# Kernel optimization log

Hardware: AMD Instinct MI355X
Metric: run time of the kernel (lower is better)

## Reference

```python
import jax, jax.numpy as jnp
import numpy as np

NUM_CLASSES = 80
STRIDE = 8
IMG_SIZE = 640
BOX_W, OBJ_W, CLS_W = 7.5, 1.0, 0.5
ANCHORS = jnp.array([[10.0, 13.0], [16.0, 30.0], [33.0, 23.0]], dtype=jnp.float32)
EPS_IOU = 1e-9
EPS_CIOU = 1e-7


def setup_inputs() -> dict:
    key = jax.random.key(0)
    k1, k2, k3 = jax.random.split(key, 3)
    B, na, H, W, D = 16, 3, 80, 80, 5 + NUM_CLASSES
    N = 48  # objects per image
    p_raw = jax.random.normal(k1, (B, na, H, W, D), dtype=jnp.float32)
    labels_xywh = jax.random.uniform(k2, (B, N, 4), dtype=jnp.float32)  # normalized (xc,yc,w,h)
    labels_cls = jax.random.randint(k3, (B, N), 0, NUM_CLASSES, dtype=jnp.int32)
    return {"p_raw": p_raw, "labels_xywh": labels_xywh, "labels_cls": labels_cls}


def _assign_targets(labels_cls, labels_xywh, B, na, H, W):
    lab = labels_xywh * IMG_SIZE  # [B,N,4] in pixels
    gx, gy, gw, gh = lab[..., 0], lab[..., 1], lab[..., 2], lab[..., 3]
    gi_idx = jnp.clip(gx / STRIDE, 0, W - 0.001).astype(jnp.int32)  # [B,N]
    gj_idx = jnp.clip(gy / STRIDE, 0, H - 0.001).astype(jnp.int32)
    a_wh = ANCHORS / STRIDE  # [na,2] anchors in grid units
    gtw, gth = gw / STRIDE, gh / STRIDE
    inter = jnp.minimum(gtw[..., None], a_wh[:, 0]) * jnp.minimum(gth[..., None], a_wh[:, 1])
    union = gtw[..., None] * gth[..., None] + a_wh[:, 0] * a_wh[:, 1] - inter + EPS_IOU
    best_a = jnp.argmax(inter / union, axis=-1).astype(jnp.int32)  # [B,N]

    # 3x3 neighborhood offsets (di over x, dj over y), matching torch loop order
    offs = jnp.array([(di, dj) for di in (-1, 0, 1) for dj in (-1, 0, 1)], dtype=jnp.int32)  # [9,2]
    bidx = jnp.arange(B, dtype=jnp.int32)

    tobj = jnp.zeros((B, na, H, W), dtype=jnp.float32)
    tcls = jnp.zeros((B, na, H, W, NUM_CLASSES), dtype=jnp.float32)
    tbox = jnp.zeros((B, na, H, W, 4), dtype=jnp.float32)

    def step(carry, x):
        tobj, tcls, tbox = carry
        a, gi, gj, c, box = x  # a,gi,gj,c: [B]; box: [B,4]
        ii = jnp.clip(gi[:, None] + offs[None, :, 0], 0, W - 1)  # [B,9]
        jj = jnp.clip(gj[:, None] + offs[None, :, 1], 0, H - 1)  # [B,9]
        b9 = jnp.broadcast_to(bidx[:, None], (B, 9))
        a9 = jnp.broadcast_to(a[:, None], (B, 9))
        c9 = jnp.broadcast_to(c[:, None], (B, 9))
        tobj = tobj.at[b9, a9, jj, ii].set(1.0)
        tcls = tcls.at[b9, a9, jj, ii, c9].set(1.0)
        tbox = tbox.at[b9, a9, jj, ii].set(jnp.broadcast_to(box[:, None, :], (B, 9, 4)))
        return (tobj, tcls, tbox), None

    xs = (best_a.T, gi_idx.T, gj_idx.T, labels_cls.T, jnp.swapaxes(lab, 0, 1))
    (tobj, tcls, tbox), _ = jax.lax.scan(step, (tobj, tcls, tbox), xs)
    return tobj, tcls, tbox


def _ciou(pred, tgt):
    # pred, tgt: [..., 4] (xc, yc, w, h) in pixels
    px, py, pw, ph = pred[..., 0], pred[..., 1], pred[..., 2], pred[..., 3]
    gx, gy, gw, gh = tgt[..., 0], tgt[..., 1], tgt[..., 2], tgt[..., 3]
    px1, py1, px2, py2 = px - pw / 2, py - ph / 2, px + pw / 2, py + ph / 2
    gx1, gy1, gx2, gy2 = gx - gw / 2, gy - gh / 2, gx + gw / 2, gy + gh / 2
    iw = jnp.clip(jnp.minimum(px2, gx2) - jnp.maximum(px1, gx1), 0)
    ih = jnp.clip(jnp.minimum(py2, gy2) - jnp.maximum(py1, gy1), 0)
    inter = iw * ih
    area_p = jnp.clip(px2 - px1, 0) * jnp.clip(py2 - py1, 0)
    area_g = jnp.clip(gx2 - gx1, 0) * jnp.clip(gy2 - gy1, 0)
    union = area_p + area_g - inter + EPS_CIOU
    iou = inter / union
    cw = jnp.clip(jnp.maximum(px2, gx2) - jnp.minimum(px1, gx1), 0)
    ch = jnp.clip(jnp.maximum(py2, gy2) - jnp.minimum(py1, gy1), 0)
    c2 = cw * cw + ch * ch + EPS_CIOU
    rho2 = (px - gx) ** 2 + (py - gy) ** 2
    v = (4.0 / (np.pi ** 2)) * (jnp.arctan(gw / (gh + EPS_CIOU)) - jnp.arctan(pw / (ph + EPS_CIOU))) ** 2
    alpha = jax.lax.stop_gradient(v / (1 - iou + v + EPS_CIOU))
    return 1 - (iou - rho2 / c2 - alpha * v)


def _bce_logits(x, t):
    # stable binary cross-entropy with logits: softplus(x) - t*x
    return jax.nn.softplus(x) - t * x


def reference(p_raw, labels_xywh, labels_cls):
    B, na, H, W, D = p_raw.shape
    ag = ANCHORS / STRIDE  # anchors in grid units
    px = jax.nn.sigmoid(p_raw[..., 0])
    py = jax.nn.sigmoid(p_raw[..., 1])
    pw = jnp.exp(p_raw[..., 2]) * ag[:, 0][None, :, None, None]
    ph = jnp.exp(p_raw[..., 3]) * ag[:, 1][None, :, None, None]
    logits_obj = p_raw[..., 4]
    logits_cls = p_raw[..., 5:]

    gyv, gxv = jnp.meshgrid(jnp.arange(H, dtype=jnp.float32), jnp.arange(W, dtype=jnp.float32), indexing='ij')
    gx = (gxv[None, None] + px) * STRIDE
    gy = (gyv[None, None] + py) * STRIDE
    pxywh = jnp.stack([gx, gy, pw * STRIDE, ph * STRIDE], -1)  # [B,na,H,W,4]

    tobj, tcls, tbox = _assign_targets(labels_cls, labels_xywh, B, na, H, W)
    pos = tobj > 0.5
    n_pos = jnp.maximum(jnp.sum(pos), 1).astype(jnp.float32)

    ciou = _ciou(pxywh, tbox)  # [B,na,H,W]
    l_box = jnp.sum(jnp.where(pos, ciou, 0.0)) / n_pos
    l_obj = jnp.mean(_bce_logits(logits_obj, tobj))
    bce_cls = _bce_logits(logits_cls, tcls)  # [B,na,H,W,nc]
    l_cls = jnp.sum(jnp.where(pos[..., None], bce_cls, 0.0)) / (n_pos * NUM_CLASSES)

    total = BOX_W * l_box + OBJ_W * l_obj + CLS_W * l_cls
    return total
```

## Files before the change

### kernel.cpp

```cpp
#include <hip/hip_runtime.h>

#define NC    80
#define B_    16
#define NA    3
#define HW    80
#define D_    85
#define NLAB  48
#define NCELL  (B_*NA*HW*HW)
#define OBJBLK 300
#define POSBLK (B_*108)
#define NBLK_T (OBJBLK+POSBLK)

__device__ __forceinline__ float softplusf(float x) {
    return fmaxf(x, 0.f) + log1pf(expf(-fabsf(x)));
}
__device__ __forceinline__ int clampi(int v, int lo, int hi) {
    return min(max(v, lo), hi);
}

__global__ __launch_bounds__(256) void k_main(const float* __restrict__ p,
                                              const float* __restrict__ lx,
                                              const int*   __restrict__ lc,
                                              float* __restrict__ opart,
                                              float* __restrict__ ppart) {
    int t = threadIdx.x, bid = blockIdx.x;
    int lane = t & 63, wid = t >> 6;
    __shared__ float r4[4][4];

    if (bid < OBJBLK) {
        int base = bid * 1024;
        const float* a0 = p + (size_t)(base + t      ) * D_ + 4;
        const float* a1 = p + (size_t)(base + t + 256) * D_ + 4;
        const float* a2 = p + (size_t)(base + t + 512) * D_ + 4;
        const float* a3 = p + (size_t)(base + t + 768) * D_ + 4;
        float x0 = *a0;
        float x1 = *a1;
        float x2 = *a2;
        float x3 = *a3;
        float s = (softplusf(x0) + softplusf(x1)) + (softplusf(x2) + softplusf(x3));
        #pragma unroll
        for (int o = 32; o; o >>= 1) s += __shfl_xor(s, o);
        if (lane == 0) r4[wid][0] = s;
        __syncthreads();
        if (t == 0) opart[bid] = r4[0][0] + r4[1][0] + r4[2][0] + r4[3][0];
        return;
    }

    int pb = bid - OBJBLK;
    int b  = pb / 108;

    __shared__ float Lgx[NLAB], Lgy[NLAB], Lgw[NLAB], Lgh[NLAB];
    __shared__ int   Lgi[NLAB], Lgj[NLAB], La[NLAB], Lc[NLAB];

    if (t < NLAB) {
        float4 L = ((const float4*)lx)[b * NLAB + t];
        float gx = L.x * 640.f, gy = L.y * 640.f;
        float gw = L.z * 640.f, gh = L.w * 640.f;
        Lgx[t] = gx; Lgy[t] = gy; Lgw[t] = gw; Lgh[t] = gh;
        Lgi[t] = (int)fminf(fmaxf(gx * 0.125f, 0.f), 79.999f);
        Lgj[t] = (int)fminf(fmaxf(gy * 0.125f, 0.f), 79.999f);
        float gtw = gw * 0.125f, gth = gh * 0.125f;
        const float aw[3] = {1.25f, 2.0f, 4.125f};
        const float ah[3] = {1.625f, 3.75f, 2.875f};
        int a = 0; float best = -1.f;
        #pragma unroll
        for (int k = 0; k < 3; k++) {
            float inter = fminf(gtw, aw[k]) * fminf(gth, ah[k]);
            float uni   = gtw * gth + aw[k] * ah[k] - inter + 1e-9f;
            float r = inter / uni;
            if (r > best) { best = r; a = k; }
        }
        La[t] = a;
        Lc[t] = lc[b * NLAB + t];
    }
    __syncthreads();

    int cand = (pb % 108) * 4 + wid;
    int n = cand / 9, off = cand % 9;
    int gi = Lgi[n], gj = Lgj[n], a = La[n];
    int ii = clampi(gi + off / 3 - 1, 0, 79);
    int jj = clampi(gj + off % 3 - 1, 0, 79);

    bool viol = false;
    if (lane < 9) {
        if (lane < off) {
            int i2 = clampi(gi + lane / 3 - 1, 0, 79);
            int j2 = clampi(gj + lane % 3 - 1, 0, 79);
            viol = (i2 == ii) && (j2 == jj);
        }
    } else {
        int n2 = n + 1 + (lane - 9);
        if (n2 < NLAB && La[n2] == a) {
            int g2 = Lgi[n2], h2 = Lgj[n2];
            viol = ii >= max(g2 - 1, 0) && ii <= min(g2 + 1, 79) &&
                   jj >= max(h2 - 1, 0) && jj <= min(h2 + 1, 79);
        }
    }
    bool own = (__ballot(viol) == 0ull);

    float box = 0.f, cls = 0.f, xc = 0.f, npf = 0.f;
    if (own) {
        int cell = ((b * NA + a) * HW + jj) * HW + ii;
        const float* pc = p + (size_t)cell * D_;
        int c = Lc[n];

        float x = pc[5 + lane];
        float cs = softplusf(x) - ((lane == c) ? x : 0.f);
        if (lane < 16) {
            float x2 = pc[69 + lane];
            cs += softplusf(x2) - ((lane + 64 == c) ? x2 : 0.f);
        }
        #pragma unroll
        for (int o = 32; o; o >>= 1) cs += __shfl_xor(cs, o);

        if (lane == 0) {
            npf = 1.f;
            cls = cs;
            xc  = pc[4];

            float awv = (a == 0) ? 10.f : ((a == 1) ? 16.f : 33.f);
            float ahv = (a == 0) ? 13.f : ((a == 1) ? 30.f : 23.f);
            float p0 = pc[0], p1 = pc[1], p2 = pc[2], p3 = pc[3];
            float sx = 1.f / (1.f + expf(-p0));
            float sy = 1.f / (1.f + expf(-p1));
            float px = ((float)ii + sx) * 8.f;
            float py = ((float)jj + sy) * 8.f;
            float pw = expf(p2) * awv;
            float ph = expf(p3) * ahv;

            float gx = Lgx[n], gy = Lgy[n], gw = Lgw[n], gh = Lgh[n];

            float px1 = px - pw * 0.5f, px2 = px + pw * 0.5f;
            float py1 = py - ph * 0.5f, py2 = py + ph * 0.5f;
            float gx1 = gx - gw * 0.5f, gx2 = gx + gw * 0.5f;
            float gy1 = gy - gh * 0.5f, gy2 = gy + gh * 0.5f;

            float iw = fmaxf(fminf(px2, gx2) - fmaxf(px1, gx1), 0.f);
            float ih = fmaxf(fminf(py2, gy2) - fmaxf(py1, gy1), 0.f);
            float inter = iw * ih;
            float ap = fmaxf(px2 - px1, 0.f) * fmaxf(py2 - py1, 0.f);
            float ag = fmaxf(gx2 - gx1, 0.f) * fmaxf(gy2 - gy1, 0.f);
            float uni = ap + ag - inter + 1e-7f;
            float iou = inter / uni;

            float cw = fmaxf(fmaxf(px2, gx2) - fminf(px1, gx1), 0.f);
            float ch = fmaxf(fmaxf(py2, gy2) - fminf(py1, gy1), 0.f);
            float c2 = cw * cw + ch * ch + 1e-7f;
            float rho2 = (px - gx) * (px - gx) + (py - gy) * (py - gy);

            float dv = atanf(gw / (gh + 1e-7f)) - atanf(pw / (ph + 1e-7f));
            float v = 0.40528473456935108577f * dv * dv;
            float alpha = v / (1.f - iou + v + 1e-7f);
            box = 1.f - (iou - rho2 / c2 - alpha * v);
        }
    }

    if (lane == 0) { r4[wid][0] = box; r4[wid][1] = cls; r4[wid][2] = xc; r4[wid][3] = npf; }
    __syncthreads();
    if (t == 0) {
        float4 o;
        o.x = r4[0][0] + r4[1][0] + r4[2][0] + r4[3][0];
        o.y = r4[0][1] + r4[1][1] + r4[2][1] + r4[3][1];
        o.z = r4[0][2] + r4[1][2] + r4[2][2] + r4[3][2];
        o.w = r4[0][3] + r4[1][3] + r4[2][3] + r4[3][3];
        ((float4*)ppart)[pb] = o;
    }
}

__global__ __launch_bounds__(256) void k_fin(const float* __restrict__ opart,
                                             const float* __restrict__ ppart,
                                             float* __restrict__ out) {
    int t = threadIdx.x, lane = t & 63, wid = t >> 6;
    float o = 0.f, box = 0.f, cls = 0.f, xc = 0.f, np = 0.f;
    if (t < OBJBLK) o = opart[t];
    #pragma unroll
    for (int k = 0; k < 7; k++) {
        int i = t + k * 256;
        if (i < POSBLK) {
            float4 v = ((const float4*)ppart)[i];
            box += v.x; cls += v.y; xc += v.z; np += v.w;
        }
    }
    #pragma unroll
    for (int s = 32; s; s >>= 1) {
        o   += __shfl_xor(o,   s);
        box += __shfl_xor(box, s);
        cls += __shfl_xor(cls, s);
        xc  += __shfl_xor(xc,  s);
        np  += __shfl_xor(np,  s);
    }
    __shared__ float r[4][5];
    if (lane == 0) { r[wid][0]=o; r[wid][1]=box; r[wid][2]=cls; r[wid][3]=xc; r[wid][4]=np; }
    __syncthreads();
    if (t == 0) {
        float O  = r[0][0] + r[1][0] + r[2][0] + r[3][0];
        float Bx = r[0][1] + r[1][1] + r[2][1] + r[3][1];
        float Cl = r[0][2] + r[1][2] + r[2][2] + r[3][2];
        float Xc = r[0][3] + r[1][3] + r[2][3] + r[3][3];
        float Np = r[0][4] + r[1][4] + r[2][4] + r[3][4];
        float npos = fmaxf(Np, 1.f);
        out[0] = 7.5f * Bx / npos
               + (O - Xc) / (float)NCELL
               + 0.5f * Cl / (npos * (float)NC);
    }
}

extern "C" void kernel_launch(void* const* d_in, const int* in_sizes, int n_in,
                              void* d_out, int out_size, void* d_ws, size_t ws_size,
                              hipStream_t stream) {
    const float* p  = (const float*)d_in[0];
    const float* lx = (const float*)d_in[1];
    const int*   lc = (const int*)d_in[2];
    float*       out = (float*)d_out;

    float* opart = (float*)d_ws;
    float* ppart = (float*)((char*)d_ws + 8192);

    k_main<<<NBLK_T, 256, 0, stream>>>(p, lx, lc, opart, ppart);
    k_fin<<<1, 256, 0, stream>>>(opart, ppart, out);
}
```

Baseline: 21.40 us.

## Fuse final reduction into main kernel via atomics and last-block finish

Removes the separate finalize kernel. Blocks now accumulate partial sums with global atomics: a double accumulator for the objectness term and float accumulators for box, class, xc and positive count. A counter lets the last block compute the output. Positive-candidate blocks are also reduced from 1728 to 432, each warp handling four candidates in a loop. This trades one kernel launch for a memset plus atomic contention, adds float-atomic order nondeterminism, and makes blocks less parallel.

```diff
diff --git a/kernel.cpp b/kernel.cpp
--- a/kernel.cpp
+++ b/kernel.cpp
@@ -8,7 +8,7 @@
 #define NLAB  48
 #define NCELL  (B_*NA*HW*HW)
 #define OBJBLK 300
-#define POSBLK (B_*108)
+#define POSBLK 432
 #define NBLK_T (OBJBLK+POSBLK)
 
 __device__ __forceinline__ float softplusf(float x) {
@@ -21,11 +21,14 @@
 __global__ __launch_bounds__(256) void k_main(const float* __restrict__ p,
                                               const float* __restrict__ lx,
                                               const int*   __restrict__ lc,
-                                              float* __restrict__ opart,
-                                              float* __restrict__ ppart) {
+                                              double* __restrict__ accd,
+                                              float*  __restrict__ accf,
+                                              int*    __restrict__ cnt,
+                                              float*  __restrict__ out) {
     int t = threadIdx.x, bid = blockIdx.x;
     int lane = t & 63, wid = t >> 6;
-    __shared__ float r4[4][4];
+
+    bool depok = false;
 
     if (bid < OBJBLK) {
         int base = bid * 1024;
@@ -37,171 +40,158 @@
         float x1 = *a1;
         float x2 = *a2;
         float x3 = *a3;
-        float s = (softplusf(x0) + softplusf(x1)) + (softplusf(x2) + softplusf(x3));
+        double s = (double)softplusf(x0) + (double)softplusf(x1)
+                 + (double)softplusf(x2) + (double)softplusf(x3);
         #pragma unroll
         for (int o = 32; o; o >>= 1) s += __shfl_xor(s, o);
-        if (lane == 0) r4[wid][0] = s;
+        __shared__ double wd[4];
+        if (lane == 0) wd[wid] = s;
         __syncthreads();
-        if (t == 0) opart[bid] = r4[0][0] + r4[1][0] + r4[2][0] + r4[3][0];
-        return;
+        if (t == 0) {
+            double s4 = wd[0] + wd[1] + wd[2] + wd[3];
+            double od = atomicAdd(accd, s4);
+            depok = (od == od);
+        }
+    } else {
+        int pb = bid - OBJBLK;
+        int b  = pb / 27, sub = pb % 27;
+
+        __shared__ float Lgx[NLAB], Lgy[NLAB], Lgw[NLAB], Lgh[NLAB];
+        __shared__ int   Lgi[NLAB], Lgj[NLAB], La[NLAB], Lc[NLAB];
+
+        if (t < NLAB) {
+            float4 L = ((const float4*)lx)[b * NLAB + t];
+            float gx = L.x * 640.f, gy = L.y * 640.f;
+            float gw = L.z * 640.f, gh = L.w * 640.f;
+            Lgx[t] = gx; Lgy[t] = gy; Lgw[t] = gw; Lgh[t] = gh;
+            Lgi[t] = (int)fminf(fmaxf(gx * 0.125f, 0.f), 79.999f);
+            Lgj[t] = (int)fminf(fmaxf(gy * 0.125f, 0.f), 79.999f);
+            float gtw = gw * 0.125f, gth = gh * 0.125f;
+            const float aw[3] = {1.25f, 2.0f, 4.125f};
+            const float ah[3] = {1.625f, 3.75f, 2.875f};
+            int a = 0; float best = -1.f;
+            #pragma unroll
+            for (int k = 0; k < 3; k++) {
+                float inter = fminf(gtw, aw[k]) * fminf(gth, ah[k]);
+                float uni   = gtw * gth + aw[k] * ah[k] - inter + 1e-9f;
+                float r = inter / uni;
+                if (r > best) { best = r; a = k; }
+            }
+            La[t] = a;
+            Lc[t] = lc[b * NLAB + t];
+        }
+        __syncthreads();
+
+        float box = 0.f, cls = 0.f, xc = 0.f, npf = 0.f;
+
+        for (int q = 0; q < 4; q++) {
+            int cand = sub * 16 + wid * 4 + q;
+            int n = cand / 9, off = cand % 9;
+            int gi = Lgi[n], gj = Lgj[n], a = La[n];
+            int ii = clampi(gi + off / 3 - 1, 0, 79);
+            int jj = clampi(gj + off % 3 - 1, 0, 79);
+
+            bool viol = false;
+            if (lane < 9) {
+                if (lane < off) {
+                    int i2 = clampi(gi + lane / 3 - 1, 0, 79);
+                    int j2 = clampi(gj + lane % 3 - 1, 0, 79);
+                    viol = (i2 == ii) && (j2 == jj);
+                }
+            } else {
+                int n2 = n + 1 + (lane - 9);
+                if (n2 < NLAB && La[n2] == a) {
+                    int g2 = Lgi[n2], h2 = Lgj[n2];
+                    viol = ii >= max(g2 - 1, 0) && ii <= min(g2 + 1, 79) &&
+                           jj >= max(h2 - 1, 0) && jj <= min(h2 + 1, 79);
+                }
+            }
+            bool own = (__ballot(viol) == 0ull);
+            if (!own) continue;
+
+            int cell = ((b * NA + a) * HW + jj) * HW + ii;
+            const float* pc = p + (size_t)cell * D_;
+            int c = Lc[n];
+
+            float x = pc[5 + lane];
+            float cs = softplusf(x) - ((lane == c) ? x : 0.f);
+            if (lane < 16) {
+                float x2 = pc[69 + lane];
+                cs += softplusf(x2) - ((lane + 64 == c) ? x2 : 0.f);
+            }
+            #pragma unroll
+            for (int o = 32; o; o >>= 1) cs += __shfl_xor(cs, o);
+
+            if (lane == 0) {
+                npf += 1.f;
+                cls += cs;
+                xc  += pc[4];
+
+                float awv = (a == 0) ? 10.f : ((a == 1) ? 16.f : 33.f);
+                float ahv = (a == 0) ? 13.f : ((a == 1) ? 30.f : 23.f);
+                float p0 = pc[0], p1 = pc[1], p2 = pc[2], p3 = pc[3];
+                float sx = 1.f / (1.f + expf(-p0));
+                float sy = 1.f / (1.f + expf(-p1));
+                float px = ((float)ii + sx) * 8.f;
+                float py = ((float)jj + sy) * 8.f;
+                float pw = expf(p2) * awv;
+                float ph = expf(p3) * ahv;
+
+                float gx = Lgx[n], gy = Lgy[n], gw = Lgw[n], gh = Lgh[n];
+
+                float px1 = px - pw * 0.5f, px2 = px + pw * 0.5f;
+                float py1 = py - ph * 0.5f, py2 = py + ph * 0.5f;
+                float gx1 = gx - gw * 0.5f, gx2 = gx + gw * 0.5f;
+                float gy1 = gy - gh * 0.5f, gy2 = gy + gh * 0.5f;
+
+                float iw = fmaxf(fminf(px2, gx2) - fmaxf(px1, gx1), 0.f);
+                float ih = fmaxf(fminf(py2, gy2) - fmaxf(py1, gy1), 0.f);
+                float inter = iw * ih;
+                float ap = fmaxf(px2 - px1, 0.f) * fmaxf(py2 - py1, 0.f);
+                float ag = fmaxf(gx2 - gx1, 0.f) * fmaxf(gy2 - gy1, 0.f);
+                float uni = ap + ag - inter + 1e-7f;
+                float iou = inter / uni;
+
+                float cw = fmaxf(fmaxf(px2, gx2) - fminf(px1, gx1), 0.f);
+                float ch = fmaxf(fmaxf(py2, gy2) - fminf(py1, gy1), 0.f);
+                float c2 = cw * cw + ch * ch + 1e-7f;
+                float rho2 = (px - gx) * (px - gx) + (py - gy) * (py - gy);
+
+                float dv = atanf(gw / (gh + 1e-7f)) - atanf(pw / (ph + 1e-7f));
+                float v = 0.40528473456935108577f * dv * dv;
+                float alpha = v / (1.f - iou + v + 1e-7f);
+                box += 1.f - (iou - rho2 / c2 - alpha * v);
+            }
+        }
+
+        __shared__ float r4[4][4];
+        if (lane == 0) { r4[wid][0]=box; r4[wid][1]=cls; r4[wid][2]=xc; r4[wid][3]=npf; }
+        __syncthreads();
+        if (t == 0) {
+            float Bx = r4[0][0]+r4[1][0]+r4[2][0]+r4[3][0];
+            float Cl = r4[0][1]+r4[1][1]+r4[2][1]+r4[3][1];
+            float Xc = r4[0][2]+r4[1][2]+r4[2][2]+r4[3][2];
+            float Np = r4[0][3]+r4[1][3]+r4[2][3]+r4[3][3];
+            float o0 = atomicAdd(&accf[0], Bx);
+            float o1 = atomicAdd(&accf[1], Cl);
+            float o2 = atomicAdd(&accf[2], Xc);
+            float o3 = atomicAdd(&accf[3], Np);
+            depok = ((o0 + o1 + o2 + o3) < 1e30f);
+        }
     }
 
-    int pb = bid - OBJBLK;
-    int b  = pb / 108;
-
-    __shared__ float Lgx[NLAB], Lgy[NLAB], Lgw[NLAB], Lgh[NLAB];
-    __shared__ int   Lgi[NLAB], Lgj[NLAB], La[NLAB], Lc[NLAB];
-
-    if (t < NLAB) {
-        float4 L = ((const float4*)lx)[b * NLAB + t];
-        float gx = L.x * 640.f, gy = L.y * 640.f;
-        float gw = L.z * 640.f, gh = L.w * 640.f;
-        Lgx[t] = gx; Lgy[t] = gy; Lgw[t] = gw; Lgh[t] = gh;
-        Lgi[t] = (int)fminf(fmaxf(gx * 0.125f, 0.f), 79.999f);
-        Lgj[t] = (int)fminf(fmaxf(gy * 0.125f, 0.f), 79.999f);
-        float gtw = gw * 0.125f, gth = gh * 0.125f;
-        const float aw[3] = {1.25f, 2.0f, 4.125f};
-        const float ah[3] = {1.625f, 3.75f, 2.875f};
-        int a = 0; float best = -1.f;
-        #pragma unroll
-        for (int k = 0; k < 3; k++) {
-            float inter = fminf(gtw, aw[k]) * fminf(gth, ah[k]);
-            float uni   = gtw * gth + aw[k] * ah[k] - inter + 1e-9f;
-            float r = inter / uni;
-            if (r > best) { best = r; a = k; }
-        }
-        La[t] = a;
-        Lc[t] = lc[b * NLAB + t];
-    }
-    __syncthreads();
-
-    int cand = (pb % 108) * 4 + wid;
-    int n = cand / 9, off = cand % 9;
-    int gi = Lgi[n], gj = Lgj[n], a = La[n];
-    int ii = clampi(gi + off / 3 - 1, 0, 79);
-    int jj = clampi(gj + off % 3 - 1, 0, 79);
-
-    bool viol = false;
-    if (lane < 9) {
-        if (lane < off) {
-            int i2 = clampi(gi + lane / 3 - 1, 0, 79);
-            int j2 = clampi(gj + lane % 3 - 1, 0, 79);
-            viol = (i2 == ii) && (j2 == jj);
-        }
-    } else {
-        int n2 = n + 1 + (lane - 9);
-        if (n2 < NLAB && La[n2] == a) {
-            int g2 = Lgi[n2], h2 = Lgj[n2];
-            viol = ii >= max(g2 - 1, 0) && ii <= min(g2 + 1, 79) &&
-                   jj >= max(h2 - 1, 0) && jj <= min(h2 + 1, 79);
-        }
-    }
-    bool own = (__ballot(viol) == 0ull);
-
-    float box = 0.f, cls = 0.f, xc = 0.f, npf = 0.f;
-    if (own) {
-        int cell = ((b * NA + a) * HW + jj) * HW + ii;
-        const float* pc = p + (size_t)cell * D_;
-        int c = Lc[n];
-
-        float x = pc[5 + lane];
-        float cs = softplusf(x) - ((lane == c) ? x : 0.f);
-        if (lane < 16) {
-            float x2 = pc[69 + lane];
-            cs += softplusf(x2) - ((lane + 64 == c) ? x2 : 0.f);
-        }
-        #pragma unroll
-        for (int o = 32; o; o >>= 1) cs += __shfl_xor(cs, o);
-
-        if (lane == 0) {
-            npf = 1.f;
-            cls = cs;
-            xc  = pc[4];
-
-            float awv = (a == 0) ? 10.f : ((a == 1) ? 16.f : 33.f);
-            float ahv = (a == 0) ? 13.f : ((a == 1) ? 30.f : 23.f);
-            float p0 = pc[0], p1 = pc[1], p2 = pc[2], p3 = pc[3];
-            float sx = 1.f / (1.f + expf(-p0));
-            float sy = 1.f / (1.f + expf(-p1));
-            float px = ((float)ii + sx) * 8.f;
-            float py = ((float)jj + sy) * 8.f;
-            float pw = expf(p2) * awv;
-            float ph = expf(p3) * ahv;
-
-            float gx = Lgx[n], gy = Lgy[n], gw = Lgw[n], gh = Lgh[n];
-
-            float px1 = px - pw * 0.5f, px2 = px + pw * 0.5f;
-            float py1 = py - ph * 0.5f, py2 = py + ph * 0.5f;
-            float gx1 = gx - gw * 0.5f, gx2 = gx + gw * 0.5f;
-            float gy1 = gy - gh * 0.5f, gy2 = gy + gh * 0.5f;
-
-            float iw = fmaxf(fminf(px2, gx2) - fmaxf(px1, gx1), 0.f);
-            float ih = fmaxf(fminf(py2, gy2) - fmaxf(py1, gy1), 0.f);
-            float inter = iw * ih;
-            float ap = fmaxf(px2 - px1, 0.f) * fmaxf(py2 - py1, 0.f);
-            float ag = fmaxf(gx2 - gx1, 0.f) * fmaxf(gy2 - gy1, 0.f);
-            float uni = ap + ag - inter + 1e-7f;
-            float iou = inter / uni;
-
-            float cw = fmaxf(fmaxf(px2, gx2) - fminf(px1, gx1), 0.f);
-            float ch = fmaxf(fmaxf(py2, gy2) - fminf(py1, gy1), 0.f);
-            float c2 = cw * cw + ch * ch + 1e-7f;
-            float rho2 = (px - gx) * (px - gx) + (py - gy) * (py - gy);
-
-            float dv = atanf(gw / (gh + 1e-7f)) - atanf(pw / (ph + 1e-7f));
-            float v = 0.40528473456935108577f * dv * dv;
-            float alpha = v / (1.f - iou + v + 1e-7f);
-            box = 1.f - (iou - rho2 / c2 - alpha * v);
-        }
-    }
-
-    if (lane == 0) { r4[wid][0] = box; r4[wid][1] = cls; r4[wid][2] = xc; r4[wid][3] = npf; }
-    __syncthreads();
-    if (t == 0) {
-        float4 o;
-        o.x = r4[0][0] + r4[1][0] + r4[2][0] + r4[3][0];
-        o.y = r4[0][1] + r4[1][1] + r4[2][1] + r4[3][1];
-        o.z = r4[0][2] + r4[1][2] + r4[2][2] + r4[3][2];
-        o.w = r4[0][3] + r4[1][3] + r4[2][3] + r4[3][3];
-        ((float4*)ppart)[pb] = o;
-    }
-}
-
-__global__ __launch_bounds__(256) void k_fin(const float* __restrict__ opart,
-                                             const float* __restrict__ ppart,
-                                             float* __restrict__ out) {
-    int t = threadIdx.x, lane = t & 63, wid = t >> 6;
-    float o = 0.f, box = 0.f, cls = 0.f, xc = 0.f, np = 0.f;
-    if (t < OBJBLK) o = opart[t];
-    #pragma unroll
-    for (int k = 0; k < 7; k++) {
-        int i = t + k * 256;
-        if (i < POSBLK) {
-            float4 v = ((const float4*)ppart)[i];
-            box += v.x; cls += v.y; xc += v.z; np += v.w;
-        }
-    }
-    #pragma unroll
-    for (int s = 32; s; s >>= 1) {
-        o   += __shfl_xor(o,   s);
-        box += __shfl_xor(box, s);
-        cls += __shfl_xor(cls, s);
-        xc  += __shfl_xor(xc,  s);
-        np  += __shfl_xor(np,  s);
-    }
-    __shared__ float r[4][5];
-    if (lane == 0) { r[wid][0]=o; r[wid][1]=box; r[wid][2]=cls; r[wid][3]=xc; r[wid][4]=np; }
-    __syncthreads();
-    if (t == 0) {
-        float O  = r[0][0] + r[1][0] + r[2][0] + r[3][0];
-        float Bx = r[0][1] + r[1][1] + r[2][1] + r[3][1];
-        float Cl = r[0][2] + r[1][2] + r[2][2] + r[3][2];
-        float Xc = r[0][3] + r[1][3] + r[2][3] + r[3][3];
-        float Np = r[0][4] + r[1][4] + r[2][4] + r[3][4];
-        float npos = fmaxf(Np, 1.f);
-        out[0] = 7.5f * Bx / npos
-               + (O - Xc) / (float)NCELL
-               + 0.5f * Cl / (npos * (float)NC);
+    if (t == 0 && depok) {
+        int tk = atomicAdd(cnt, 1);
+        if (tk == NBLK_T - 1) {
+            double O  = atomicAdd(accd, 0.0);
+            float Bx = atomicAdd(&accf[0], 0.f);
+            float Cl = atomicAdd(&accf[1], 0.f);
+            float Xc = atomicAdd(&accf[2], 0.f);
+            float Np = atomicAdd(&accf[3], 0.f);
+            float npos = fmaxf(Np, 1.f);
+            float lobj = (float)((O - (double)Xc) / (double)NCELL);
+            out[0] = 7.5f * Bx / npos + lobj + 0.5f * Cl / (npos * (float)NC);
+        }
     }
 }
 
@@ -213,9 +203,10 @@
     const int*   lc = (const int*)d_in[2];
     float*       out = (float*)d_out;
 
-    float* opart = (float*)d_ws;
-    float* ppart = (float*)((char*)d_ws + 8192);
-
-    k_main<<<NBLK_T, 256, 0, stream>>>(p, lx, lc, opart, ppart);
-    k_fin<<<1, 256, 0, stream>>>(opart, ppart, out);
-}
+    double* accd = (double*)d_ws;
+    float*  accf = (float*)((char*)d_ws + 8);
+    int*    cnt  = (int*)((char*)d_ws + 24);
+
+    hipMemsetAsync(d_ws, 0, 32, stream);
+    k_main<<<NBLK_T, 256, 0, stream>>>(p, lx, lc, accd, accf, cnt, out);
+}
```

After: 51.76 us. 142% more time.
